# Kernel tuning notes

Hardware: AMD Instinct MI355X
Metric: run time of the kernel (lower is better)

## Reference

```python
import jax, jax.numpy as jnp
import numpy as np

BATCH, SEQ, DIMS, HEADS = 4, 2048, 1024, 16
HEAD_DIM = DIMS // HEADS          # 64
ROT = HEAD_DIM // 2               # 32
BASE = 10000.0


def setup_inputs() -> dict:
    key = jax.random.key(0)
    k1, k2, k3, k4 = jax.random.split(key, 4)
    x = jax.random.normal(k1, (BATCH, SEQ, DIMS), jnp.float32)
    thetas = jax.random.normal(k2, (ROT,), jnp.float32) * 0.02
    theta_scale = jnp.ones((1,), jnp.float32)
    # nn.init.orthogonal_ equivalent
    a = jax.random.normal(k3, (HEAD_DIM, HEAD_DIM), jnp.float32)
    r_matrix, _ = jnp.linalg.qr(a)
    inv_freq = 1.0 / (BASE ** (jnp.arange(0, HEAD_DIM, 2, dtype=jnp.float32) / HEAD_DIM))
    # r_pairs: torch rand(rot,2)*head_dim then .long() -> ints in [0, head_dim)
    pairs = jax.random.randint(k4, (ROT, 2), 0, HEAD_DIM, dtype=jnp.int32)
    return {"x": x, "thetas": thetas, "theta_scale": theta_scale,
            "r_matrix": r_matrix, "inv_freq": inv_freq, "pairs": pairs}


def _forward(x, thetas, theta_scale, r_matrix, inv_freq, pairs):
    B, S, D = x.shape
    hd = r_matrix.shape[0]
    H = D // hd
    ts = theta_scale[0]
    xf = x.reshape(-1, hd)  # (B*S*H, hd)

    # Sequential Givens rotations: x @ G_k, applied as 2-column updates.
    # G[i,i]=c, G[j,j]=c, G[i,j]=-s, G[j,i]=s. If i==j, sequential torch
    def body(xx, k):
        i, j = pairs[k, 0], pairs[k, 1]
        th = thetas[k] * ts
        c, s = jnp.cos(th), jnp.sin(th)
        xi = xx[:, i]
        xj = xx[:, j]
        ni = xi * c + xj * s
        nj = jnp.where(i == j, xi * s, xj * c - xi * s)
        xx = xx.at[:, i].set(ni)
        xx = xx.at[:, j].set(nj)  # overwrites column i when i == j
        return xx, None

    xf, _ = jax.lax.scan(body, xf, jnp.arange(pairs.shape[0]))
    xf = xf @ r_matrix
    xh = xf.reshape(B, S, H, hd)

    # rotary sin/cos encoding (concatenated halves, not interleaved)
    pos = jnp.arange(S, dtype=x.dtype)[:, None]          # (S, 1)
    si = pos * inv_freq[None, :]                          # (S, hd//2)
    sin = jnp.sin(si)[None, :, None, :]                   # (1, S, 1, hd//2)
    cos = jnp.cos(si)[None, :, None, :]
    x1, x2 = xh[..., ::2], xh[..., 1::2]
    out = jnp.concatenate([x1 * cos - x2 * sin, x1 * sin + x2 * cos], axis=-1)
    return out.reshape(B, S, D) * jnp.sqrt(jnp.asarray(D, x.dtype))


def reference(x, thetas, theta_scale, r_matrix, inv_freq, pairs):
    return _forward(x, thetas, theta_scale, r_matrix, inv_freq, pairs)
```

## Files before the change

### kernel.cpp

```cpp
#include <hip/hip_runtime.h>
#include <math.h>

#define SEQ    2048
#define ROT    32
#define ROWS_PER_BLOCK 128
#define NTILES (131072 / ROWS_PER_BLOCK)

__global__ __launch_bounds__(256) void build_w_kernel(
    const float* __restrict__ thetas,
    const float* __restrict__ theta_scale,
    const float* __restrict__ R,
    const int*   __restrict__ pairs,
    float*       __restrict__ W)
{
    __shared__ float A[64 * 65];
    const int t = threadIdx.x;

    #pragma unroll
    for (int i = 0; i < 16; ++i) {
        int e = i * 256 + t;
        int r = e >> 6, c = e & 63;
        A[r * 65 + c] = (r == c) ? 1.0f : 0.0f;
    }
    __syncthreads();

    if (t < 64) {
        const float ts = theta_scale[0];
        float* Ar = &A[t * 65];
        for (int k = 0; k < ROT; ++k) {
            int i = pairs[2 * k], j = pairs[2 * k + 1];
            float th = thetas[k] * ts;
            float c = cosf(th), s = sinf(th);
            float ai = Ar[i], aj = Ar[j];
            if (i != j) { Ar[i] = c * ai + s * aj; Ar[j] = c * aj - s * ai; }
            else        { Ar[i] = s * ai; }
        }
    }
    __syncthreads();

    const int r = (blockIdx.x << 2) + (t >> 6);
    const int c = t & 63;
    const float* Ar = &A[r * 65];
    float acc = 0.0f;
    #pragma unroll 8
    for (int k = 0; k < 64; ++k)
        acc = fmaf(Ar[k], R[k * 64 + c], acc);
    W[r * 64 + c] = 32.0f * acc;
}

__global__ __launch_bounds__(256) void rotary_main_kernel(
    const float* __restrict__ x,
    const float* __restrict__ W,
    const float* __restrict__ inv_freq,
    float*       __restrict__ out)
{
    __shared__ float Xt[64 * 128];
    __shared__ float Ws[64 * 64];
    __shared__ float SCc[8 * 32];
    __shared__ float SCs[8 * 32];

    const int T = blockIdx.x;
    const int t = threadIdx.x;

    const float4* xg = (const float4*)(x + (size_t)T * (ROWS_PER_BLOCK * 64));
    #pragma unroll
    for (int it = 0; it < 8; ++it) {
        int g = it * 256 + t;
        float4 v = xg[g];
        int row = g >> 4;
        int k4  = (g & 15) << 2;
        float vv[4] = {v.x, v.y, v.z, v.w};
        #pragma unroll
        for (int j = 0; j < 4; ++j) {
            int k = k4 + j;
            Xt[k * 128 + (((row >> 2) ^ (k & 31)) << 2) + (row & 3)] = vv[j];
        }
    }
    {
        const float4* wg  = (const float4*)W;
        float4*       ws4 = (float4*)Ws;
        #pragma unroll
        for (int i = 0; i < 4; ++i)
            ws4[i * 256 + t] = wg[i * 256 + t];
    }
    {
        int pg = t >> 5, d = t & 31;
        int pos = (T * 8 + pg) & (SEQ - 1);
        float sv, cv;
        sincosf((float)pos * inv_freq[d], &sv, &cv);
        SCc[t] = cv;
        SCs[t] = sv;
    }
    __syncthreads();

    const int rg = t >> 3;
    const int cg = t & 7;

    float acc[4][8];
    #pragma unroll
    for (int m = 0; m < 4; ++m)
        #pragma unroll
        for (int j = 0; j < 8; ++j) acc[m][j] = 0.0f;

    #pragma unroll 4
    for (int k = 0; k < 64; ++k) {
        const float4 xv = *(const float4*)&Xt[k * 128 + ((rg ^ (k & 31)) << 2)];
        const float4 w0 = *(const float4*)&Ws[k * 64 + cg * 8];
        const float4 w1 = *(const float4*)&Ws[k * 64 + cg * 8 + 4];
        const float xs[4] = {xv.x, xv.y, xv.z, xv.w};
        const float ws[8] = {w0.x, w0.y, w0.z, w0.w, w1.x, w1.y, w1.z, w1.w};
        #pragma unroll
        for (int m = 0; m < 4; ++m)
            #pragma unroll
            for (int j = 0; j < 8; ++j)
                acc[m][j] = fmaf(xs[m], ws[j], acc[m][j]);
    }

    const int scb = (rg >> 2) * 32 + cg * 4;
    const float4 cv = *(const float4*)&SCc[scb];
    const float4 sv = *(const float4*)&SCs[scb];
    const float cs4[4] = {cv.x, cv.y, cv.z, cv.w};
    const float sn4[4] = {sv.x, sv.y, sv.z, sv.w};

    float* og = out + (size_t)T * (ROWS_PER_BLOCK * 64);
    #pragma unroll
    for (int m = 0; m < 4; ++m) {
        int row = rg * 4 + m;
        float o1[4], o2[4];
        #pragma unroll
        for (int d = 0; d < 4; ++d) {
            float a = acc[m][2 * d];
            float b = acc[m][2 * d + 1];
            o1[d] = a * cs4[d] - b * sn4[d];
            o2[d] = a * sn4[d] + b * cs4[d];
        }
        *(float4*)&og[row * 64 + cg * 4]      = make_float4(o1[0], o1[1], o1[2], o1[3]);
        *(float4*)&og[row * 64 + 32 + cg * 4] = make_float4(o2[0], o2[1], o2[2], o2[3]);
    }
}

extern "C" void kernel_launch(void* const* d_in, const int* in_sizes, int n_in,
                              void* d_out, int out_size, void* d_ws, size_t ws_size,
                              hipStream_t stream) {
    const float* x           = (const float*)d_in[0];
    const float* thetas      = (const float*)d_in[1];
    const float* theta_scale = (const float*)d_in[2];
    const float* r_matrix    = (const float*)d_in[3];
    const float* inv_freq    = (const float*)d_in[4];
    const int*   pairs       = (const int*)d_in[5];
    float*       out         = (float*)d_out;
    float*       W           = (float*)d_ws;

    build_w_kernel<<<16, 256, 0, stream>>>(thetas, theta_scale, r_matrix, pairs, W);
    rotary_main_kernel<<<NTILES, 256, 0, stream>>>(x, W, inv_freq, out);
}
```

Baseline: 112.7 us.

## Load x and W directly into LDS with global_load_lds and row-major swizzle

Replaces the register-staged transposed store of x into shared memory with asynchronous global-to-LDS 16-byte loads into a row-major, XOR-swizzled tile. W is loaded the same way. The inner product loop is restructured to read four-row float4 slices of x and four W rows per step, which changes LDS access patterns. This removes VGPR staging and the scattered scalar LDS writes, but it relies on the compiler inserting the correct waits before the barrier.

```diff
diff --git a/kernel.cpp b/kernel.cpp
--- a/kernel.cpp
+++ b/kernel.cpp
@@ -5,6 +5,9 @@
 #define ROT    32
 #define ROWS_PER_BLOCK 128
 #define NTILES (131072 / ROWS_PER_BLOCK)
+
+#define AS1 __attribute__((address_space(1)))
+#define AS3 __attribute__((address_space(3)))
 
 __global__ __launch_bounds__(256) void build_w_kernel(
     const float* __restrict__ thetas,
@@ -54,34 +57,34 @@
     const float* __restrict__ inv_freq,
     float*       __restrict__ out)
 {
-    __shared__ float Xt[64 * 128];
+    __shared__ float Xs[128 * 64];
     __shared__ float Ws[64 * 64];
     __shared__ float SCc[8 * 32];
     __shared__ float SCs[8 * 32];
 
-    const int T = blockIdx.x;
-    const int t = threadIdx.x;
+    const int T    = blockIdx.x;
+    const int t    = threadIdx.x;
+    const int wave = t >> 6;
+    const int lane = t & 63;
 
-    const float4* xg = (const float4*)(x + (size_t)T * (ROWS_PER_BLOCK * 64));
+    const float* xg = x + (size_t)T * (ROWS_PER_BLOCK * 64);
+
     #pragma unroll
-    for (int it = 0; it < 8; ++it) {
-        int g = it * 256 + t;
-        float4 v = xg[g];
-        int row = g >> 4;
-        int k4  = (g & 15) << 2;
-        float vv[4] = {v.x, v.y, v.z, v.w};
-        #pragma unroll
-        for (int j = 0; j < 4; ++j) {
-            int k = k4 + j;
-            Xt[k * 128 + (((row >> 2) ^ (k & 31)) << 2) + (row & 3)] = vv[j];
-        }
+    for (int i = 0; i < 8; ++i) {
+        int ri  = i * 4 + wave;
+        int row = ri * 4 + (lane >> 4);
+        int q   = (lane & 15) ^ (ri & 7);
+        const float* gp = xg + row * 64 + q * 4;
+        __builtin_amdgcn_global_load_lds((const AS1 unsigned int*)gp,
+                                         (AS3 unsigned int*)&Xs[ri * 256], 16, 0, 0);
     }
-    {
-        const float4* wg  = (const float4*)W;
-        float4*       ws4 = (float4*)Ws;
-        #pragma unroll
-        for (int i = 0; i < 4; ++i)
-            ws4[i * 256 + t] = wg[i * 256 + t];
+    #pragma unroll
+    for (int i = 0; i < 4; ++i) {
+        int ri  = i * 4 + wave;
+        int row = ri * 4 + (lane >> 4);
+        const float* gp = W + row * 64 + (lane & 15) * 4;
+        __builtin_amdgcn_global_load_lds((const AS1 unsigned int*)gp,
+                                         (AS3 unsigned int*)&Ws[ri * 256], 16, 0, 0);
     }
     {
         int pg = t >> 5, d = t & 31;
@@ -102,18 +105,35 @@
         #pragma unroll
         for (int j = 0; j < 8; ++j) acc[m][j] = 0.0f;
 
-    #pragma unroll 4
-    for (int k = 0; k < 64; ++k) {
-        const float4 xv = *(const float4*)&Xt[k * 128 + ((rg ^ (k & 31)) << 2)];
-        const float4 w0 = *(const float4*)&Ws[k * 64 + cg * 8];
-        const float4 w1 = *(const float4*)&Ws[k * 64 + cg * 8 + 4];
-        const float xs[4] = {xv.x, xv.y, xv.z, xv.w};
-        const float ws[8] = {w0.x, w0.y, w0.z, w0.w, w1.x, w1.y, w1.z, w1.w};
+    const int xslot = (rg & 7);
+    #pragma unroll 2
+    for (int kk = 0; kk < 16; ++kk) {
+        float4 xv[4];
         #pragma unroll
         for (int m = 0; m < 4; ++m)
+            xv[m] = *(const float4*)&Xs[(rg * 4 + m) * 64 + ((kk ^ xslot) << 2)];
+        float4 wv[8];
+        #pragma unroll
+        for (int r = 0; r < 4; ++r) {
+            wv[2 * r]     = *(const float4*)&Ws[(4 * kk + r) * 64 + cg * 8];
+            wv[2 * r + 1] = *(const float4*)&Ws[(4 * kk + r) * 64 + cg * 8 + 4];
+        }
+        #pragma unroll
+        for (int m = 0; m < 4; ++m) {
+            const float xs4[4] = {xv[m].x, xv[m].y, xv[m].z, xv[m].w};
             #pragma unroll
-            for (int j = 0; j < 8; ++j)
-                acc[m][j] = fmaf(xs[m], ws[j], acc[m][j]);
+            for (int r = 0; r < 4; ++r) {
+                const float4 w0 = wv[2 * r], w1 = wv[2 * r + 1];
+                acc[m][0] = fmaf(xs4[r], w0.x, acc[m][0]);
+                acc[m][1] = fmaf(xs4[r], w0.y, acc[m][1]);
+                acc[m][2] = fmaf(xs4[r], w0.z, acc[m][2]);
+                acc[m][3] = fmaf(xs4[r], w0.w, acc[m][3]);
+                acc[m][4] = fmaf(xs4[r], w1.x, acc[m][4]);
+                acc[m][5] = fmaf(xs4[r], w1.y, acc[m][5]);
+                acc[m][6] = fmaf(xs4[r], w1.z, acc[m][6]);
+                acc[m][7] = fmaf(xs4[r], w1.w, acc[m][7]);
+            }
+        }
     }
 
     const int scb = (rg >> 2) * 32 + cg * 4;
```

New measurement: 112.4 us. Within noise of the previous version (-0.2%).
